# Optimization experiments

Measured on AMD Instinct MI355X. Metric: run time of the kernel, lower is better.

Reference implementation:

```python
import jax, jax.numpy as jnp
import numpy as np

N = 50000
E = 800000
IN_FEATS = 256
NUM_HEADS = 4
OUT_FEATS = 64
NUM_ETYPES = 8
ALPHA = 100.0
NEG_SLOPE_ATTN = 0.2   # self.leaky_relu
NEG_SLOPE_EW = 0.01    # nn.LeakyReLU() default, applied to edge weights


def leaky_relu(x, slope):
    return jnp.where(x >= 0, x, slope * x)


def setup_inputs() -> dict:
    key = jax.random.key(0)
    ks = jax.random.split(key, 8)
    feat = jax.random.normal(ks[0], (N, IN_FEATS), dtype=jnp.float32)
    src = jax.random.randint(ks[1], (E,), 0, N, dtype=jnp.int32)
    dst = jax.random.randint(ks[2], (E,), 0, N, dtype=jnp.int32)
    # etypes are 1-indexed in the original code (edge_weight[edge_feats - 1])
    edge_feats = jax.random.randint(ks[3], (E,), 1, NUM_ETYPES + 1, dtype=jnp.int32)
    # parameters (xavier-normal-ish init for weights; edge_weight = 1/alpha)
    fc_w = jax.random.normal(ks[4], (NUM_HEADS * OUT_FEATS, IN_FEATS), dtype=jnp.float32) * 0.05
    attn_l = jax.random.normal(ks[5], (1, NUM_HEADS, OUT_FEATS), dtype=jnp.float32) * 0.1
    attn_r = jax.random.normal(ks[6], (1, NUM_HEADS, OUT_FEATS), dtype=jnp.float32) * 0.1
    edge_weight = jnp.full((NUM_ETYPES, NUM_HEADS), 1.0 / ALPHA, dtype=jnp.float32)
    return {"feat": feat, "src": src, "dst": dst, "edge_feats": edge_feats,
            "fc_w": fc_w, "attn_l": attn_l, "attn_r": attn_r, "edge_weight": edge_weight}


def reference(feat, src, dst, edge_feats, fc_w, attn_l, attn_r, edge_weight):
    # feat: [N, F_in] -> ft: [N, H, D]
    ft = (feat @ fc_w.T).reshape(-1, NUM_HEADS, OUT_FEATS)
    el = jnp.einsum('nhd,ohd->nh', ft, attn_l)  # [N, H]
    er = jnp.einsum('nhd,ohd->nh', ft, attn_r)  # [N, H]
    # edge-type weights (1-indexed), scaled & leaky-relu'd
    ew = leaky_relu(edge_weight * ALPHA, NEG_SLOPE_EW)  # [T, H]
    ee = ew[edge_feats - 1]                              # [E, H]
    # per-edge logits: u_add_v, times edge weight, leaky relu
    e = leaky_relu((el[src] + er[dst]) * ee, NEG_SLOPE_ATTN)  # [E, H]
    # edge softmax grouped by destination node
    emax = jax.ops.segment_max(e, dst, num_segments=N)        # [N, H]
    ex = jnp.exp(e - emax[dst])
    denom = jax.ops.segment_sum(ex, dst, num_segments=N)      # [N, H]
    a = ex / denom[dst]                                        # [E, H]
    # weighted scatter-sum: sum over edges of a * ft[src]
    msg = ft[src] * a[:, :, None]                              # [E, H, D]
    rst = jax.ops.segment_sum(msg, dst, num_segments=N)       # [N, H, D]
    return rst
```

## Files before the change

### kernel.cpp

```cpp
#include <hip/hip_runtime.h>
#include <hip/hip_bf16.h>


#define NF 256
#define HD 256
#define NH 4

typedef __attribute__((ext_vector_type(8))) short short8;
typedef __attribute__((ext_vector_type(4))) float f32x4;

static __device__ __forceinline__ unsigned short f2bf(float f) {
  unsigned int u = __float_as_uint(f);
  u += 0x7FFFu + ((u >> 16) & 1u);
  return (unsigned short)(u >> 16);
}
static __device__ __forceinline__ float bf2f(unsigned short s) {
  return __uint_as_float(((unsigned int)s) << 16);
}
static __device__ __forceinline__ unsigned pkbf(float a, float b) {
  __hip_bfloat162 h = __float22bfloat162_rn(make_float2(a, b));
  return *(unsigned*)&h;
}
static __device__ __forceinline__ float wcalc(float sum, float ew) {
  float x = sum * ew;
  x = (x >= 0.f) ? x : 0.2f * x;
  return __expf(x);
}

__global__ __launch_bounds__(256) void init_k(
    const float* __restrict__ w, unsigned short* __restrict__ o,
    int* __restrict__ cursor, int n) {
  int i = blockIdx.x * 256 + threadIdx.x;
  if (i < 16384) {
    float4 v = ((const float4*)w)[i];
    ((uint2*)o)[i] = make_uint2(pkbf(v.x, v.y), pkbf(v.z, v.w));
  }
  int nq = n >> 2;
  if (i < nq) ((int4*)cursor)[i] = make_int4(0, 0, 0, 0);
  int t = nq * 4 + i;
  if (i < (n & 3)) cursor[t] = 0;
}

__global__ __launch_bounds__(256) void gemm_hist_k(
    const float* __restrict__ feat, const unsigned short* __restrict__ fcb,
    const float* __restrict__ attn_l, const float* __restrict__ attn_r,
    unsigned short* __restrict__ ftb, float* __restrict__ el,
    float* __restrict__ er, int n,
    const int* __restrict__ src, const int* __restrict__ dst,
    const int* __restrict__ efeats, int* __restrict__ cursor,
    int* __restrict__ rkw, int e, int gb, int hb) {
  __shared__ short aF[4 * 2 * 64 * 8];
  __shared__ short bF[16 * 2 * 64 * 8];

  if (blockIdx.x >= gb) {
    int stride = hb * 256;
    for (int i = (blockIdx.x - gb) * 256 + threadIdx.x; i < e; i += stride) {
      int r = atomicAdd(&cursor[dst[i]], 1);
      rkw[i] = src[i] | ((efeats[i] - 1) << 17) | (r << 20);
    }
    return;
  }

  int tid = threadIdx.x;
  int lane = tid & 63, w = tid >> 6;
  int row0 = blockIdx.x * 64;

  f32x4 acc[4][4];
#pragma unroll
  for (int i = 0; i < 4; ++i)
#pragma unroll
    for (int j = 0; j < 4; ++j) acc[i][j] = (f32x4){0.f, 0.f, 0.f, 0.f};

  int ar = tid >> 2, ak = (tid & 3) << 4;
  int arow = row0 + ar; if (arow >= n) arow = n - 1;
  const float* ap = feat + (size_t)arow * NF + ak;
  int am = ar & 15, art = ar >> 4;
  int s0 = ak >> 5, q0 = (ak >> 3) & 3;
  int s1 = (ak + 8) >> 5, q1 = ((ak + 8) >> 3) & 3;
  short* aw0 = &aF[(((art * 2 + s0) * 64) + q0 * 16 + am) * 8];
  short* aw1 = &aF[(((art * 2 + s1) * 64) + q1 * 16 + am) * 8];

  const unsigned short* bp = fcb + (size_t)tid * NF;
  int bn = tid & 15, bcg = tid >> 4;

  for (int k0 = 0; k0 < NF; k0 += 64) {
    float4 f0 = *(const float4*)(ap + k0);
    float4 f1 = *(const float4*)(ap + k0 + 4);
    float4 f2 = *(const float4*)(ap + k0 + 8);
    float4 f3 = *(const float4*)(ap + k0 + 12);
    uint4 oa = make_uint4(pkbf(f0.x, f0.y), pkbf(f0.z, f0.w),
                          pkbf(f1.x, f1.y), pkbf(f1.z, f1.w));
    uint4 ob = make_uint4(pkbf(f2.x, f2.y), pkbf(f2.z, f2.w),
                          pkbf(f3.x, f3.y), pkbf(f3.z, f3.w));
    *(uint4*)aw0 = oa;
    *(uint4*)aw1 = ob;
#pragma unroll
    for (int o8 = 0; o8 < 8; ++o8) {
      short8 bv = *(const short8*)(bp + k0 + o8 * 8);
      int bs = o8 >> 2, bq = o8 & 3;
      *(short8*)&bF[(((bcg * 2 + bs) * 64) + bq * 16 + bn) * 8] = bv;
    }
    __syncthreads();
#pragma unroll
    for (int s = 0; s < 2; ++s) {
      short8 af[4], bfr[4];
#pragma unroll
      for (int rt = 0; rt < 4; ++rt)
        af[rt] = *(const short8*)&aF[(((rt * 2 + s) * 64) + lane) * 8];
#pragma unroll
      for (int ct = 0; ct < 4; ++ct)
        bfr[ct] = *(const short8*)&bF[((((w * 4 + ct) * 2 + s) * 64) + lane) * 8];
#pragma unroll
      for (int rt = 0; rt < 4; ++rt)
#pragma unroll
        for (int ct = 0; ct < 4; ++ct)
          acc[rt][ct] = __builtin_amdgcn_mfma_f32_16x16x32_bf16(
              af[rt], bfr[ct], acc[rt][ct], 0, 0, 0);
    }
    __syncthreads();
  }

  int ln = lane & 15, lq = lane >> 4;
  float al4[4], ar4[4];
#pragma unroll
  for (int ct = 0; ct < 4; ++ct) {
    al4[ct] = attn_l[w * 64 + ct * 16 + ln];
    ar4[ct] = attn_r[w * 64 + ct * 16 + ln];
  }
#pragma unroll
  for (int rt = 0; rt < 4; ++rt) {
#pragma unroll
    for (int r = 0; r < 4; ++r) {
      float pl = 0.f, pr = 0.f;
#pragma unroll
      for (int ct = 0; ct < 4; ++ct) {
        float v = acc[rt][ct][r];
        pl += v * al4[ct]; pr += v * ar4[ct];
      }
#pragma unroll
      for (int off = 1; off <= 8; off <<= 1) {
        pl += __shfl_xor(pl, off);
        pr += __shfl_xor(pr, off);
      }
      int row = row0 + rt * 16 + lq * 4 + r;
      if (row < n) {
        if (ln == 0) { el[row * NH + w] = pl; er[row * NH + w] = pr; }
        unsigned short* fr = ftb + (size_t)row * HD + w * 64 + ln;
#pragma unroll
        for (int ct = 0; ct < 4; ++ct) fr[ct * 16] = f2bf(acc[rt][ct][r]);
      }
    }
  }
}

__global__ __launch_bounds__(1024) void scan_k(const int* __restrict__ cursor,
                                               int* __restrict__ poffs, int n) {
  __shared__ int wtot[16];
  __shared__ int wexcl[16];
  __shared__ int ctot;
  int tid = threadIdx.x, lane = tid & 63, wid = tid >> 6;
  int carry = 0;
  int nchunk = (n + 8191) >> 13;
  for (int c = 0; c < nchunk; ++c) {
    int base = (c << 13) + tid * 8;
    int v[8];
    if (base + 8 <= n) {
      int4 a = *(const int4*)(cursor + base);
      int4 b = *(const int4*)(cursor + base + 4);
      v[0] = a.x; v[1] = a.y; v[2] = a.z; v[3] = a.w;
      v[4] = b.x; v[5] = b.y; v[6] = b.z; v[7] = b.w;
    } else {
#pragma unroll
      for (int j = 0; j < 8; ++j) v[j] = (base + j < n) ? cursor[base + j] : 0;
    }
#pragma unroll
    for (int j = 0; j < 8; ++j) v[j] = (v[j] + 7) & ~7;
    int p[8]; int run = 0;
#pragma unroll
    for (int j = 0; j < 8; ++j) { run += v[j]; p[j] = run; }
    int incl = run;
#pragma unroll
    for (int off = 1; off < 64; off <<= 1) {
      int t = __shfl_up(incl, off);
      if (lane >= off) incl += t;
    }
    if (lane == 63) wtot[wid] = incl;
    __syncthreads();
    if (wid == 0 && lane < 16) {
      int wv = wtot[lane]; int wi = wv;
#pragma unroll
      for (int off = 1; off < 16; off <<= 1) {
        int t = __shfl_up(wi, off);
        if (lane >= off) wi += t;
      }
      wexcl[lane] = wi - wv;
      if (lane == 15) ctot = wi;
    }
    __syncthreads();
    int ebase = carry + wexcl[wid] + (incl - run);
#pragma unroll
    for (int j = 0; j < 8; ++j) {
      int i = base + j;
      if (i < n) poffs[i] = ebase + p[j] - v[j];
    }
    carry += ctot;
    __syncthreads();
  }
  if (tid == 0) poffs[n] = carry;
}

__global__ __launch_bounds__(256) void pack_k(
    const int* __restrict__ dst, const int* __restrict__ rkw,
    const int* __restrict__ poffs, int* __restrict__ pk, int e) {
  int i = blockIdx.x * 256 + threadIdx.x;
  if (i >= e) return;
  unsigned v = (unsigned)rkw[i];
  int p = poffs[dst[i]] + (int)(v >> 20);
  pk[p] = (int)(v & 0xFFFFFu);
}

__global__ __launch_bounds__(256) void agg4_k(
    const unsigned short* __restrict__ ftb, const int* __restrict__ pk,
    const float* __restrict__ el, const float* __restrict__ er,
    const float* __restrict__ ewt, const int* __restrict__ poffs,
    const int* __restrict__ cnt, float* __restrict__ out, int n) {
  __shared__ float ew_s[32];
  if (threadIdx.x < 32) {
    float v = ewt[threadIdx.x] * 100.0f;
    ew_s[threadIdx.x] = (v >= 0.f) ? v : 0.01f * v;
  }
  __syncthreads();
  int node = blockIdx.x * 4 + (threadIdx.x >> 6);
  int lane = threadIdx.x & 63;
  if (node >= n) return;
  int start = poffs[node];
  int deg = cnt[node];
  float o0 = 0.f, o1 = 0.f, o2 = 0.f, o3 = 0.f;
  if (deg > 0) {
    int hl = lane >> 4;
    float er_h = er[(size_t)node * NH + hl];
    const unsigned short* fb = ftb + (size_t)lane * 4;
    const float* elh = el + hl;
    const int* pg = pk + start;
    float ss = 0.f;
    int ng = (deg + 7) >> 3;
    int4 pa = *(const int4*)(pg);
    int4 pb = *(const int4*)(pg + 4);
    for (int g = 0; g < ng; ++g) {
      int4 na = *(const int4*)(pg + (g + 1) * 8);
      int4 nb = *(const int4*)(pg + (g + 1) * 8 + 4);
      int rem = deg - (g << 3);
      if (rem < 8) {
        pa.y = (rem > 1) ? pa.y : 0;
        pa.z = (rem > 2) ? pa.z : 0;
        pa.w = (rem > 3) ? pa.w : 0;
        pb.x = (rem > 4) ? pb.x : 0;
        pb.y = (rem > 5) ? pb.y : 0;
        pb.z = (rem > 6) ? pb.z : 0;
        pb.w = (rem > 7) ? pb.w : 0;
      }
      int sA = pa.x & 0x1FFFF, tA = pa.x >> 17;
      int sB = pa.y & 0x1FFFF, tB = pa.y >> 17;
      int sC = pa.z & 0x1FFFF, tC = pa.z >> 17;
      int sD = pa.w & 0x1FFFF, tD = pa.w >> 17;
      int sE = pb.x & 0x1FFFF, tE = pb.x >> 17;
      int sF = pb.y & 0x1FFFF, tF = pb.y >> 17;
      int sG = pb.z & 0x1FFFF, tG = pb.z >> 17;
      int sH = pb.w & 0x1FFFF, tH = pb.w >> 17;
      float eA = elh[sA * NH], eB = elh[sB * NH], eC = elh[sC * NH], eD = elh[sD * NH];
      float eE = elh[sE * NH], eF = elh[sF * NH], eG = elh[sG * NH], eH = elh[sH * NH];
      ushort4 fA = *(const ushort4*)(fb + (size_t)sA * HD);
      ushort4 fB = *(const ushort4*)(fb + (size_t)sB * HD);
      ushort4 fC = *(const ushort4*)(fb + (size_t)sC * HD);
      ushort4 fD = *(const ushort4*)(fb + (size_t)sD * HD);
      ushort4 fE = *(const ushort4*)(fb + (size_t)sE * HD);
      ushort4 fF = *(const ushort4*)(fb + (size_t)sF * HD);
      ushort4 fG = *(const ushort4*)(fb + (size_t)sG * HD);
      ushort4 fH = *(const ushort4*)(fb + (size_t)sH * HD);
      float wA = wcalc(eA + er_h, ew_s[tA * NH + hl]);
      float wB = wcalc(eB + er_h, ew_s[tB * NH + hl]);
      float wC = wcalc(eC + er_h, ew_s[tC * NH + hl]);
      float wD = wcalc(eD + er_h, ew_s[tD * NH + hl]);
      float wE = wcalc(eE + er_h, ew_s[tE * NH + hl]);
      float wF = wcalc(eF + er_h, ew_s[tF * NH + hl]);
      float wG = wcalc(eG + er_h, ew_s[tG * NH + hl]);
      float wH = wcalc(eH + er_h, ew_s[tH * NH + hl]);
      if (rem < 8) {
        wB = (rem > 1) ? wB : 0.f;
        wC = (rem > 2) ? wC : 0.f;
        wD = (rem > 3) ? wD : 0.f;
        wE = (rem > 4) ? wE : 0.f;
        wF = (rem > 5) ? wF : 0.f;
        wG = (rem > 6) ? wG : 0.f;
        wH = (rem > 7) ? wH : 0.f;
      }
      ss += ((wA + wB) + (wC + wD)) + ((wE + wF) + (wG + wH));
      o0 = fmaf(wA, bf2f(fA.x), o0); o1 = fmaf(wA, bf2f(fA.y), o1);
      o2 = fmaf(wA, bf2f(fA.z), o2); o3 = fmaf(wA, bf2f(fA.w), o3);
      o0 = fmaf(wB, bf2f(fB.x), o0); o1 = fmaf(wB, bf2f(fB.y), o1);
      o2 = fmaf(wB, bf2f(fB.z), o2); o3 = fmaf(wB, bf2f(fB.w), o3);
      o0 = fmaf(wC, bf2f(fC.x), o0); o1 = fmaf(wC, bf2f(fC.y), o1);
      o2 = fmaf(wC, bf2f(fC.z), o2); o3 = fmaf(wC, bf2f(fC.w), o3);
      o0 = fmaf(wD, bf2f(fD.x), o0); o1 = fmaf(wD, bf2f(fD.y), o1);
      o2 = fmaf(wD, bf2f(fD.z), o2); o3 = fmaf(wD, bf2f(fD.w), o3);
      o0 = fmaf(wE, bf2f(fE.x), o0); o1 = fmaf(wE, bf2f(fE.y), o1);
      o2 = fmaf(wE, bf2f(fE.z), o2); o3 = fmaf(wE, bf2f(fE.w), o3);
      o0 = fmaf(wF, bf2f(fF.x), o0); o1 = fmaf(wF, bf2f(fF.y), o1);
      o2 = fmaf(wF, bf2f(fF.z), o2); o3 = fmaf(wF, bf2f(fF.w), o3);
      o0 = fmaf(wG, bf2f(fG.x), o0); o1 = fmaf(wG, bf2f(fG.y), o1);
      o2 = fmaf(wG, bf2f(fG.z), o2); o3 = fmaf(wG, bf2f(fG.w), o3);
      o0 = fmaf(wH, bf2f(fH.x), o0); o1 = fmaf(wH, bf2f(fH.y), o1);
      o2 = fmaf(wH, bf2f(fH.z), o2); o3 = fmaf(wH, bf2f(fH.w), o3);
      pa = na; pb = nb;
    }
    float rs = 1.0f / ss;
    o0 *= rs; o1 *= rs; o2 *= rs; o3 *= rs;
  }
  *(float4*)(out + (size_t)node * HD + lane * 4) = make_float4(o0, o1, o2, o3);
}

extern "C" void kernel_launch(void* const* d_in, const int* in_sizes, int n_in,
                              void* d_out, int out_size, void* d_ws, size_t ws_size,
                              hipStream_t stream) {
  const float* feat   = (const float*)d_in[0];
  const int*   src    = (const int*)d_in[1];
  const int*   dst    = (const int*)d_in[2];
  const int*   efeats = (const int*)d_in[3];
  const float* fc_w   = (const float*)d_in[4];
  const float* attn_l = (const float*)d_in[5];
  const float* attn_r = (const float*)d_in[6];
  const float* ewt    = (const float*)d_in[7];
  float* out = (float*)d_out;

  int N = in_sizes[0] / NF;
  int E = in_sizes[1];

  char* ws = (char*)d_ws;
  size_t off = 0;
  unsigned short* fcb = (unsigned short*)(ws + off); off += (size_t)NF * HD * 2;
  unsigned short* ftb = (unsigned short*)(ws + off); off += (size_t)N * HD * 2;
  float* el  = (float*)(ws + off);  off += (size_t)N * NH * 4;
  float* er  = (float*)(ws + off);  off += (size_t)N * NH * 4;
  int* poffs = (int*)(ws + off);    off += ((size_t)N + 16) * 4;
  int* cursor = (int*)(ws + off);   off += (size_t)N * 4;
  int* rkw   = (int*)(ws + off);    off += (size_t)E * 4;
  int* pk    = (int*)(ws + off);    off += ((size_t)E + 7 * (size_t)N + 64) * 4;

  int gblocks = (N + 63) / 64;
  int hblocks = 1024 - gblocks;
  if (hblocks < 64) hblocks = 64;

  init_k<<<64, 256, 0, stream>>>(fc_w, fcb, cursor, N);
  gemm_hist_k<<<gblocks + hblocks, 256, 0, stream>>>(
      feat, fcb, attn_l, attn_r, ftb, el, er, N,
      src, dst, efeats, cursor, rkw, E, gblocks, hblocks);
  scan_k<<<1, 1024, 0, stream>>>(cursor, poffs, N);
  pack_k<<<(E + 255) / 256, 256, 0, stream>>>(dst, rkw, poffs, pk, E);
  agg4_k<<<(N + 3) / 4, 256, 0, stream>>>(ftb, pk, el, er, ewt, poffs, cursor, out, N);
}
```

Before: 275.4 us.

## Split per-node degree counters into four sub-counters to reduce atomic contention

Each destination node's counter becomes four int counters selected by edge index mod 4, which spreads atomicAdd contention across addresses. The rank packing is reorganised to hold a 2-bit sub-counter id plus a 10-bit rank, and the scan, pack and aggregation kernels sum the int4 to get the degree and derive each sub-bucket's offset. The histogram blocks are also placed before the GEMM blocks in the launch order so they get scheduled first. In exchange, the counter array is four times larger and more memory is read during the scan and pack, and the rank field is now limited to 10 bits.

```diff
diff --git a/kernel.cpp b/kernel.cpp
--- a/kernel.cpp
+++ b/kernel.cpp
@@ -29,16 +29,13 @@
 
 __global__ __launch_bounds__(256) void init_k(
     const float* __restrict__ w, unsigned short* __restrict__ o,
-    int* __restrict__ cursor, int n) {
+    int4* __restrict__ cursor4, int n) {
   int i = blockIdx.x * 256 + threadIdx.x;
   if (i < 16384) {
     float4 v = ((const float4*)w)[i];
     ((uint2*)o)[i] = make_uint2(pkbf(v.x, v.y), pkbf(v.z, v.w));
   }
-  int nq = n >> 2;
-  if (i < nq) ((int4*)cursor)[i] = make_int4(0, 0, 0, 0);
-  int t = nq * 4 + i;
-  if (i < (n & 3)) cursor[t] = 0;
+  for (int q = i; q < n; q += 64 * 256) cursor4[q] = make_int4(0, 0, 0, 0);
 }
 
 __global__ __launch_bounds__(256) void gemm_hist_k(
@@ -48,22 +45,25 @@
     float* __restrict__ er, int n,
     const int* __restrict__ src, const int* __restrict__ dst,
     const int* __restrict__ efeats, int* __restrict__ cursor,
-    int* __restrict__ rkw, int e, int gb, int hb) {
+    unsigned* __restrict__ rkw, int e, int hb) {
   __shared__ short aF[4 * 2 * 64 * 8];
   __shared__ short bF[16 * 2 * 64 * 8];
 
-  if (blockIdx.x >= gb) {
+  if (blockIdx.x < hb) {
     int stride = hb * 256;
-    for (int i = (blockIdx.x - gb) * 256 + threadIdx.x; i < e; i += stride) {
-      int r = atomicAdd(&cursor[dst[i]], 1);
-      rkw[i] = src[i] | ((efeats[i] - 1) << 17) | (r << 20);
+    for (int i = blockIdx.x * 256 + threadIdx.x; i < e; i += stride) {
+      int d = dst[i];
+      unsigned r = (unsigned)i & 3u;
+      unsigned rk = (unsigned)atomicAdd(&cursor[((unsigned)d << 2) | r], 1);
+      rkw[i] = (unsigned)src[i] | (((unsigned)efeats[i] - 1u) << 17) |
+               (r << 20) | (rk << 22);
     }
     return;
   }
 
   int tid = threadIdx.x;
   int lane = tid & 63, w = tid >> 6;
-  int row0 = blockIdx.x * 64;
+  int row0 = (blockIdx.x - hb) * 64;
 
   f32x4 acc[4][4];
 #pragma unroll
@@ -153,7 +153,7 @@
   }
 }
 
-__global__ __launch_bounds__(1024) void scan_k(const int* __restrict__ cursor,
+__global__ __launch_bounds__(1024) void scan_k(const int4* __restrict__ cursor4,
                                                int* __restrict__ poffs, int n) {
   __shared__ int wtot[16];
   __shared__ int wexcl[16];
@@ -164,14 +164,13 @@
   for (int c = 0; c < nchunk; ++c) {
     int base = (c << 13) + tid * 8;
     int v[8];
-    if (base + 8 <= n) {
-      int4 a = *(const int4*)(cursor + base);
-      int4 b = *(const int4*)(cursor + base + 4);
-      v[0] = a.x; v[1] = a.y; v[2] = a.z; v[3] = a.w;
-      v[4] = b.x; v[5] = b.y; v[6] = b.z; v[7] = b.w;
-    } else {
-#pragma unroll
-      for (int j = 0; j < 8; ++j) v[j] = (base + j < n) ? cursor[base + j] : 0;
+#pragma unroll
+    for (int j = 0; j < 8; ++j) {
+      int i = base + j;
+      if (i < n) {
+        int4 c4 = cursor4[i];
+        v[j] = c4.x + c4.y + c4.z + c4.w;
+      } else v[j] = 0;
     }
 #pragma unroll
     for (int j = 0; j < 8; ++j) v[j] = (v[j] + 7) & ~7;
@@ -210,20 +209,26 @@
 }
 
 __global__ __launch_bounds__(256) void pack_k(
-    const int* __restrict__ dst, const int* __restrict__ rkw,
-    const int* __restrict__ poffs, int* __restrict__ pk, int e) {
+    const int* __restrict__ dst, const unsigned* __restrict__ rkw,
+    const int* __restrict__ poffs, const int4* __restrict__ cursor4,
+    int* __restrict__ pk, int e) {
   int i = blockIdx.x * 256 + threadIdx.x;
   if (i >= e) return;
-  unsigned v = (unsigned)rkw[i];
-  int p = poffs[dst[i]] + (int)(v >> 20);
-  pk[p] = (int)(v & 0xFFFFFu);
+  unsigned v = rkw[i];
+  int d = dst[i];
+  unsigned r = (v >> 20) & 3u;
+  unsigned rk = v >> 22;
+  int4 c4 = cursor4[d];
+  int base = poffs[d] + ((r > 0) ? c4.x : 0) + ((r > 1) ? c4.y : 0) +
+             ((r > 2) ? c4.z : 0);
+  pk[base + (int)rk] = (int)(v & 0xFFFFFu);
 }
 
 __global__ __launch_bounds__(256) void agg4_k(
     const unsigned short* __restrict__ ftb, const int* __restrict__ pk,
     const float* __restrict__ el, const float* __restrict__ er,
     const float* __restrict__ ewt, const int* __restrict__ poffs,
-    const int* __restrict__ cnt, float* __restrict__ out, int n) {
+    const int4* __restrict__ cursor4, float* __restrict__ out, int n) {
   __shared__ float ew_s[32];
   if (threadIdx.x < 32) {
     float v = ewt[threadIdx.x] * 100.0f;
@@ -234,7 +239,8 @@
   int lane = threadIdx.x & 63;
   if (node >= n) return;
   int start = poffs[node];
-  int deg = cnt[node];
+  int4 c4 = cursor4[node];
+  int deg = c4.x + c4.y + c4.z + c4.w;
   float o0 = 0.f, o1 = 0.f, o2 = 0.f, o3 = 0.f;
   if (deg > 0) {
     int hl = lane >> 4;
@@ -342,19 +348,20 @@
   float* el  = (float*)(ws + off);  off += (size_t)N * NH * 4;
   float* er  = (float*)(ws + off);  off += (size_t)N * NH * 4;
   int* poffs = (int*)(ws + off);    off += ((size_t)N + 16) * 4;
-  int* cursor = (int*)(ws + off);   off += (size_t)N * 4;
-  int* rkw   = (int*)(ws + off);    off += (size_t)E * 4;
+  int* cursor = (int*)(ws + off);   off += (size_t)N * 16;
+  unsigned* rkw = (unsigned*)(ws + off); off += (size_t)E * 4;
   int* pk    = (int*)(ws + off);    off += ((size_t)E + 7 * (size_t)N + 64) * 4;
 
   int gblocks = (N + 63) / 64;
   int hblocks = 1024 - gblocks;
   if (hblocks < 64) hblocks = 64;
 
-  init_k<<<64, 256, 0, stream>>>(fc_w, fcb, cursor, N);
+  init_k<<<64, 256, 0, stream>>>(fc_w, fcb, (int4*)cursor, N);
   gemm_hist_k<<<gblocks + hblocks, 256, 0, stream>>>(
       feat, fcb, attn_l, attn_r, ftb, el, er, N,
-      src, dst, efeats, cursor, rkw, E, gblocks, hblocks);
-  scan_k<<<1, 1024, 0, stream>>>(cursor, poffs, N);
-  pack_k<<<(E + 255) / 256, 256, 0, stream>>>(dst, rkw, poffs, pk, E);
-  agg4_k<<<(N + 3) / 4, 256, 0, stream>>>(ftb, pk, el, er, ewt, poffs, cursor, out, N);
-}
+      src, dst, efeats, cursor, rkw, E, hblocks);
+  scan_k<<<1, 1024, 0, stream>>>((const int4*)cursor, poffs, N);
+  pack_k<<<(E + 255) / 256, 256, 0, stream>>>(dst, rkw, poffs, (const int4*)cursor, pk, E);
+  agg4_k<<<(N + 3) / 4, 256, 0, stream>>>(ftb, pk, el, er, ewt, poffs,
+                                          (const int4*)cursor, out, N);
+}
```

Measured after the change: 288.4 us. 4.7% more time.
